# Performance work log

Measured on AMD Instinct MI355X. Metric: run time of the kernel, lower is better.

Reference implementation:

```python
import jax, jax.numpy as jnp
import numpy as np

B, N, D, CI, CO = 16, 1024, 16, 128, 128
ITERS = 3
EPS_BN = 1e-5
EPS_SQ = 1e-8


def sparsemax(z, axis):
    # Martins & Astudillo sparsemax along `axis`.
    K = z.shape[axis]
    z_s = jnp.flip(jnp.sort(z, axis=axis), axis=axis)  # descending
    z_cum = jnp.cumsum(z_s, axis=axis)
    shp = [1] * z.ndim
    shp[axis] = K
    k = jnp.arange(1, K + 1, dtype=z.dtype).reshape(shp)
    support = 1.0 + k * z_s > z_cum
    k_z = jnp.sum(support, axis=axis, keepdims=True).astype(z.dtype)
    tau_sum = jnp.sum(jnp.where(support, z_s, 0.0), axis=axis, keepdims=True)
    tau = (tau_sum - 1.0) / k_z
    return jnp.maximum(z - tau, 0.0)


def squash(s, axis):
    sq = jnp.sum(s * s, axis=axis, keepdims=True)
    return (sq / (1.0 + sq)) * s / jnp.sqrt(sq + EPS_SQ)


def setup_inputs() -> dict:
    key = jax.random.key(0)
    ks = jax.random.split(key, 4)
    x = jax.random.normal(ks[0], (B, N, CI), jnp.float32)
    a = jax.random.uniform(ks[1], (B, N, N), jnp.float32)
    adj = (a < 0.02).astype(jnp.float32)
    adj = jnp.maximum(adj, jnp.swapaxes(adj, -1, -2))  # symmetric 0/1 adjacency
    bn_gamma = jnp.ones((CI,), jnp.float32)
    bn_beta = jnp.zeros((CI,), jnp.float32)
    W = jax.random.normal(ks[2], (D, CI, CO), jnp.float32) / np.sqrt(CI)
    bias = jnp.zeros((D, CO), jnp.float32)
    return {"x": x, "adj": adj, "bn_gamma": bn_gamma, "bn_beta": bn_beta,
            "W": W, "bias": bias}


def _forward(x, adj, bn_gamma, bn_beta, W, bias):
    # BatchNorm1d, training-mode batch stats over flattened [B*N, CI]
    xf = x.reshape(-1, x.shape[-1])
    mu = xf.mean(0)
    var = ((xf - mu) ** 2).mean(0)  # biased variance (torch BN normalization)
    xn = (x - mu) / jnp.sqrt(var + EPS_BN) * bn_gamma + bn_beta

    # DenseGCNConv per digit capsule; adjacency normalization is shared.
    n = adj.shape[-1]
    eye = jnp.eye(n, dtype=adj.dtype)
    a = adj * (1.0 - eye) + eye                    # diag set to 1 (self-loops)
    dis = jnp.clip(a.sum(-1), 1.0, None) ** -0.5
    a_norm = dis[:, :, None] * a * dis[:, None, :]  # D^-1/2 A D^-1/2
    xw = jnp.einsum('bni,dio->bndo', xn, W)
    u = jnp.einsum('bmn,bndo->bmdo', a_norm, xw) + bias  # u_hat [B,N,D,CO]

    u_det = jax.lax.stop_gradient(u)  # torch uses u_hat.detach() in the loop
    b = jnp.zeros(u.shape[:3], u.dtype)  # [B,N,D]
    for _ in range(ITERS - 1):
        c = sparsemax(b, axis=2)
        s = jnp.einsum('bnd,bndo->bdo', c, u_det)
        v = squash(s, axis=-1)  # squash over capsule dim (dim=-2 in torch view)
        b = b + jnp.einsum('bndo,bdo->bnd', u_det, v)

    c = sparsemax(b, axis=2)
    s = jnp.einsum('bnd,bndo->bdo', c, u)
    s = s + xn.mean(1)[:, None, :]  # residual; broadcasts over D (needs CI==CO)
    # Original squashes with dim=-1 over a trailing singleton -> elementwise squash
    sq = s * s
    v = (sq / (1.0 + sq)) * s / jnp.sqrt(sq + EPS_SQ)

    adj_out = jnp.einsum('bnd,bnm,bme->bde', c, adj, c)  # coarsened adjacency
    return v, adj_out


def reference(x, adj, bn_gamma, bn_beta, W, bias):
    return _forward(x, adj, bn_gamma, bn_beta, W, bias)
```

## Files before the change

### kernel.cpp

```cpp
#include <hip/hip_runtime.h>

#define NB 16
#define NN 1024
#define ND 16
#define NCI 128
#define NCO 128
#define BN_ROWS (NB*NN)
#define MAXDEG 128
#define VOFF_ADJ (NB*ND*NCO)

__device__ __forceinline__ void fma4(float4& a, float s, const float4& w) {
    a.x = fmaf(s, w.x, a.x); a.y = fmaf(s, w.y, a.y);
    a.z = fmaf(s, w.z, a.z); a.w = fmaf(s, w.w, a.w);
}
__device__ __forceinline__ void add4(float4& a, const float4& b) {
    a.x += b.x; a.y += b.y; a.z += b.z; a.w += b.w;
}

__global__ __launch_bounds__(256) void k_pre1(const float* __restrict__ x,
                                              float* __restrict__ pbn,
                                              const float* __restrict__ W,
                                              float* __restrict__ Wt) {
    __shared__ float4 ls[8][32], lq[8][32];
    __shared__ float tile[32][33];
    int t = threadIdx.x;
    if (blockIdx.x < 256) {
        int q = t & 31, rg = t >> 5;
        int row0 = blockIdx.x * 64;
        const float4* x4 = (const float4*)x;
        float4 s = make_float4(0, 0, 0, 0), sq = make_float4(0, 0, 0, 0);
        for (int r = rg; r < 64; r += 8) {
            float4 v = x4[(size_t)(row0 + r) * 32 + q];
            s.x += v.x; s.y += v.y; s.z += v.z; s.w += v.w;
            sq.x = fmaf(v.x, v.x, sq.x); sq.y = fmaf(v.y, v.y, sq.y);
            sq.z = fmaf(v.z, v.z, sq.z); sq.w = fmaf(v.w, v.w, sq.w);
        }
        ls[rg][q] = s; lq[rg][q] = sq;
        __syncthreads();
        if (t < 32) {
            float4 a = ls[0][t];
            #pragma unroll
            for (int r = 1; r < 8; ++r) add4(a, ls[r][t]);
            ((float4*)(pbn + (size_t)blockIdx.x * 256))[t] = a;
        } else if (t < 64) {
            int qq = t - 32;
            float4 a = lq[0][qq];
            #pragma unroll
            for (int r = 1; r < 8; ++r) add4(a, lq[r][qq]);
            ((float4*)(pbn + (size_t)blockIdx.x * 256 + 128))[qq] = a;
        }
    } else {
        int d = blockIdx.x - 256;
        int r = t >> 5, cq = t & 31;
        const float* Wd = W + (size_t)d * NCI * NCO;
        float* Wtd = Wt + (size_t)d * NCI * NCO;
        for (int ti = 0; ti < 4; ++ti)
            for (int tj = 0; tj < 4; ++tj) {
                __syncthreads();
                for (int rr = r; rr < 32; rr += 8)
                    tile[rr][cq] = Wd[(size_t)(ti * 32 + rr) * 128 + tj * 32 + cq];
                __syncthreads();
                for (int rr = r; rr < 32; rr += 8)
                    Wtd[(size_t)(tj * 32 + rr) * 128 + ti * 32 + cq] = tile[cq][rr];
            }
    }
}

__global__ __launch_bounds__(256) void k_pre2(const float* __restrict__ adj,
        float* __restrict__ dis, int* __restrict__ nbr_idx, int* __restrict__ nbr_cnt,
        float* __restrict__ selfd, const float* __restrict__ pbn,
        const float* __restrict__ gamma, const float* __restrict__ beta,
        float* __restrict__ ss, float* __restrict__ xm) {
    int t = threadIdx.x;
    if (blockIdx.x < NB * NN) {
        int bm = blockIdx.x;
        int m = bm & (NN - 1);
        const float4* row4 = (const float4*)(adj + (size_t)bm * NN);
        __shared__ int cnt;
        __shared__ int idx[MAXDEG];
        if (t == 0) { cnt = 1; idx[0] = m; }
        __syncthreads();
        float4 v = row4[t];
        int n0 = t * 4;
        float av[4] = {v.x, v.y, v.z, v.w};
        #pragma unroll
        for (int j = 0; j < 4; ++j) {
            int n = n0 + j;
            if (n == m) {
                selfd[bm] = (av[j] > 0.5f) ? 1.f : 0.f;
            } else if (av[j] > 0.5f) {
                int p = atomicAdd(&cnt, 1);
                if (p < MAXDEG) idx[p] = n;
            }
        }
        __syncthreads();
        int c = min(cnt, MAXDEG);
        if (t == 0) {
            nbr_cnt[bm] = c;
            dis[bm] = rsqrtf((float)c);
        }
        for (int k = t; k < c; k += 256) nbr_idx[(size_t)bm * MAXDEG + k] = idx[k];
    } else {
        int b = blockIdx.x - NB * NN;
        if (t < 128) {
            float s = 0.f, sq = 0.f, sb = 0.f;
            for (int blk = 0; blk < 256; ++blk) {
                float v = pbn[(size_t)blk * 256 + t];
                s += v;
                sq += pbn[(size_t)blk * 256 + 128 + t];
                sb += ((blk >> 4) == b) ? v : 0.f;
            }
            float mu = s * (1.f / BN_ROWS);
            float var = sq * (1.f / BN_ROWS) - mu * mu;
            float sc = gamma[t] * rsqrtf(var + 1e-5f);
            float sh = beta[t] - mu * sc;
            if (b == 0) { ss[t] = sc; ss[128 + t] = sh; }
            xm[b * NCI + t] = sb * (1.f / NN) * sc + sh;
        }
    }
}

__global__ void k_y(const float* __restrict__ x, const float* __restrict__ ss,
                    const float* __restrict__ dis, const int* __restrict__ nbr_idx,
                    const int* __restrict__ nbr_cnt, float* __restrict__ y) {
    int l = blockIdx.x;
    int idx0 = l >> 3;
    int b = (l & 7) + ((idx0 >> 10) << 3);
    int m = idx0 & 1023;
    int bm = (b << 10) + m;
    int t = threadIdx.x;
    int q = t & 31, ng = t >> 5;
    __shared__ float sw[MAXDEG];
    __shared__ int sIdx[MAXDEG];
    int cnt = nbr_cnt[bm];
    float dm = dis[bm];
    for (int k = t; k < cnt; k += 128) {
        int n = nbr_idx[(size_t)bm * MAXDEG + k];
        sIdx[k] = n;
        sw[k] = dm * dis[(b << 10) + n];
    }
    __syncthreads();
    const float4* xb = (const float4*)(x + ((size_t)(b << 10)) * NCI);
    float4 acc = make_float4(0, 0, 0, 0);
    float wsum = 0.f;
    for (int k = ng; k < cnt; k += 4) {
        float w = sw[k];
        float4 v = xb[(size_t)sIdx[k] * 32 + q];
        fma4(acc, w, v);
        wsum += w;
    }
    __shared__ float4 lacc[4][32];
    __shared__ float lws[4];
    lacc[ng][q] = acc;
    if (q == 0) lws[ng] = wsum;
    __syncthreads();
    if (t < 32) {
        float4 a = lacc[0][t];
        add4(a, lacc[1][t]); add4(a, lacc[2][t]); add4(a, lacc[3][t]);
        float wst = lws[0] + lws[1] + lws[2] + lws[3];
        float4 sc = ((const float4*)ss)[t];
        float4 sh = ((const float4*)(ss + 128))[t];
        float4 o;
        o.x = sc.x * a.x + sh.x * wst;
        o.y = sc.y * a.y + sh.y * wst;
        o.z = sc.z * a.z + sh.z * wst;
        o.w = sc.w * a.w + sh.w * wst;
        ((float4*)(y + (size_t)bm * NCI))[t] = o;
    }
}

__device__ __forceinline__ void sv_phase(int b, int d, int t, int mode,
    const float* __restrict__ gsrc, const float* __restrict__ pcs,
    const float* __restrict__ W, const float* __restrict__ Wt,
    const float* __restrict__ bias, const float* __restrict__ xm,
    float* __restrict__ hbuf, float* __restrict__ hbb, float* __restrict__ outv,
    float* gl, float4 (*red)[32], float* redf, float* svec, float* vvv,
    float* csum_s, float* scal)
{
    if (mode == 0) {
        int q = t & 31, rg = t >> 5;
        const float4* yb = (const float4*)(gsrc + (((size_t)b) << 10) * NCI);
        float4 s = make_float4(0, 0, 0, 0);
        #pragma unroll 4
        for (int r = rg; r < 1024; r += 8) add4(s, yb[(size_t)r * 32 + q]);
        red[rg][q] = s;
        if (t == 0) *csum_s = 64.f;
        __syncthreads();
        if (t < 32) {
            float4 a = red[0][t];
            #pragma unroll
            for (int r = 1; r < 8; ++r) add4(a, red[r][t]);
            a.x *= (1.f / 16.f); a.y *= (1.f / 16.f);
            a.z *= (1.f / 16.f); a.w *= (1.f / 16.f);
            ((float4*)gl)[t] = a;
        }
        __syncthreads();
    } else {
        int col = t & 127, half = t >> 7;
        float g = 0.f;
        #pragma unroll 4
        for (int ch = half * 16; ch < half * 16 + 16; ++ch)
            g += gsrc[(((size_t)b * 32 + ch) * 16 + d) * NCI + col];
        ((float*)red)[half * 128 + col] = g;
        if (t == 0) {
            float cs = 0.f;
            #pragma unroll
            for (int ch = 0; ch < 32; ++ch) cs += pcs[(b * 32 + ch) * 16 + d];
            *csum_s = cs;
        }
        __syncthreads();
        if (t < 128) gl[t] = ((float*)red)[t] + ((float*)red)[128 + t];
        __syncthreads();
    }

    {
        int q = t & 31, hh = t >> 5;
        const float4* Wd4 = (const float4*)(W + (size_t)d * NCI * NCO);
        float4 acc = make_float4(0, 0, 0, 0);
        for (int i = hh * 16; i < hh * 16 + 16; ++i)
            fma4(acc, gl[i], Wd4[(size_t)i * 32 + q]);
        red[hh][q] = acc;
    }
    __syncthreads();
    if (t < 32) {
        float4 a = red[0][t];
        #pragma unroll
        for (int r = 1; r < 8; ++r) add4(a, red[r][t]);
        float4 b4 = ((const float4*)(bias + d * NCO))[t];
        float cs = *csum_s;
        a.x = fmaf(cs, b4.x, a.x); a.y = fmaf(cs, b4.y, a.y);
        a.z = fmaf(cs, b4.z, a.z); a.w = fmaf(cs, b4.w, a.w);
        ((float4*)svec)[t] = a;
    }
    __syncthreads();

    if (mode == 2) {
        if (t < 128) {
            float sv2 = svec[t] + xm[b * NCO + t];
            float sq = sv2 * sv2;
            outv[(size_t)(b * 16 + d) * NCO + t] = (sq / (1.f + sq)) * sv2 * rsqrtf(sq + 1e-8f);
        }
        return;
    }

    redf[t] = (t < 128) ? svec[t] * svec[t] : 0.f;
    __syncthreads();
    if (t < 64) {
        float val = redf[t] + redf[t + 64] + redf[t + 128] + redf[t + 192];
        #pragma unroll
        for (int m2 = 32; m2 >= 1; m2 >>= 1) val += __shfl_xor(val, m2);
        if (t == 0) *scal = val;
    }
    __syncthreads();
    if (t < 128) {
        float tot = *scal;
        vvv[t] = (tot / (1.f + tot)) * svec[t] * rsqrtf(tot + 1e-8f);
    }
    __syncthreads();

    {
        int q = t & 31, hh = t >> 5;
        const float4* Wt4 = (const float4*)(Wt + (size_t)d * NCI * NCO);
        float4 acc = make_float4(0, 0, 0, 0);
        for (int o = hh * 16; o < hh * 16 + 16; ++o)
            fma4(acc, vvv[o], Wt4[(size_t)o * 32 + q]);
        red[hh][q] = acc;
    }
    redf[t] = (t < 128) ? bias[d * NCO + t] * vvv[t] : 0.f;
    __syncthreads();
    if (t < 32) {
        float4 a = red[0][t];
        #pragma unroll
        for (int r = 1; r < 8; ++r) add4(a, red[r][t]);
        ((float4*)(hbuf + (size_t)(b * 16 + d) * NCI))[t] = a;
    }
    if (t >= 64 && t < 128) {
        int tt = t - 64;
        float val = redf[tt] + redf[tt + 64] + redf[tt + 128] + redf[tt + 192];
        #pragma unroll
        for (int m2 = 32; m2 >= 1; m2 >>= 1) val += __shfl_xor(val, m2);
        if (tt == 0) hbb[b * 16 + d] = val;
    }
}

__global__ __launch_bounds__(256) void k_sv(const float* __restrict__ gsrc,
        const float* __restrict__ pcs, const float* __restrict__ W,
        const float* __restrict__ Wt, const float* __restrict__ bias,
        const float* __restrict__ xm, float* __restrict__ hbuf,
        float* __restrict__ hbb, float* __restrict__ outv, int mode) {
    __shared__ float gl[128], svec[128], vvv[128];
    __shared__ float4 red[8][32];
    __shared__ float redf[256];
    __shared__ float csum_s, scal;
    int l = blockIdx.x, idx0 = l >> 3;
    int b = (l & 7) + ((idx0 >> 4) << 3);
    int d = idx0 & 15;
    sv_phase(b, d, threadIdx.x, mode, gsrc, pcs, W, Wt, bias, xm,
             hbuf, hbb, outv, gl, red, redf, svec, vvv, &csum_s, &scal);
}

__global__ __launch_bounds__(256) void k_bgc(const float* __restrict__ y,
        const float* __restrict__ hbuf, const float* __restrict__ hbb,
        float* __restrict__ blog, float* __restrict__ cglob,
        float* __restrict__ pg, float* __restrict__ pcs,
        float* __restrict__ outz, int first, int last) {
    int l = blockIdx.x, idx0 = l >> 3;
    int b = (l & 7) + ((idx0 >> 5) << 3);
    int j = idx0 & 31;
    int t = threadIdx.x;
    int n0 = j * 32;
    __shared__ __align__(16) float sy[32 * 128];
    __shared__ __align__(16) float sh[16 * 132];
    __shared__ float shb[16];
    __shared__ float scd[32][17];
    {
        const float4* hb4 = (const float4*)(hbuf + (size_t)b * 16 * NCI);
        float4* sh4 = (float4*)sh;
        for (int jj = t; jj < 16 * 32; jj += 256) {
            int row = jj >> 5, col = jj & 31;
            sh4[row * 33 + col] = hb4[row * 32 + col];
        }
        const float4* yb4 = (const float4*)(y + (((size_t)b << 10) + n0) * NCI);
        float4* sy4 = (float4*)sy;
        for (int jj = t; jj < 32 * 32; jj += 256) sy4[jj] = yb4[jj];
        if (t < 16) shb[t] = hbb[b * 16 + t];
    }
    __syncthreads();
    int nsub = t >> 4, d = t & 15;
    #pragma unroll
    for (int nn = nsub; nn < 32; nn += 16) {
        float acc = 0.f;
        const float* yr = &sy[nn * 128];
        const float* hr = &sh[d * 132];
        #pragma unroll 8
        for (int i = 0; i < 128; i += 4) {
            float4 a = *(const float4*)&yr[i];
            float4 h4 = *(const float4*)&hr[i];
            acc = fmaf(a.x, h4.x, acc);
            acc = fmaf(a.y, h4.y, acc);
            acc = fmaf(a.z, h4.z, acc);
            acc = fmaf(a.w, h4.w, acc);
        }
        size_t idx = (((size_t)b << 10) + n0 + nn) * ND + d;
        float bnew = acc + shb[d] + (first ? 0.f : blog[idx]);
        if (!last) blog[idx] = bnew;
        scd[nn][d] = bnew;
    }
    __syncthreads();
    if (t < 32) {
        float z[16], zs[16];
        #pragma unroll
        for (int d2 = 0; d2 < 16; ++d2) { z[d2] = scd[t][d2]; zs[d2] = z[d2]; }
        #pragma unroll
        for (int a = 0; a < 16; ++a) {
            #pragma unroll
            for (int b2 = a + 1; b2 < 16; ++b2) {
                float hi = fmaxf(zs[a], zs[b2]);
                float lo = fminf(zs[a], zs[b2]);
                zs[a] = hi; zs[b2] = lo;
            }
        }
        float cs = 0.f, tausum = 0.f;
        int kz = 1;
        #pragma unroll
        for (int k = 1; k <= 16; ++k) {
            cs += zs[k - 1];
            if (1.f + (float)k * zs[k - 1] > cs) { kz = k; tausum = cs; }
        }
        float tau = (tausum - 1.f) / (float)kz;
        #pragma unroll
        for (int d2 = 0; d2 < 16; ++d2) scd[t][d2] = fmaxf(z[d2] - tau, 0.f);
    }
    __syncthreads();
    if (last) {
        for (int jj = t; jj < 32 * 16; jj += 256)
            cglob[(((size_t)b << 10) + n0 + (jj >> 4)) * ND + (jj & 15)] = scd[jj >> 4][jj & 15];
        if (j == 0) outz[VOFF_ADJ + b * 256 + t] = 0.f;
    }
    if (t < 16) {
        float cs = 0.f;
        #pragma unroll 4
        for (int nn = 0; nn < 32; ++nn) cs += scd[nn][t];
        pcs[(b * 32 + j) * 16 + t] = cs;
    }
    int col = t & 127, dh = t >> 7;
    float accg[8] = {};
    for (int nn = 0; nn < 32; ++nn) {
        float yv = sy[nn * 128 + col];
        #pragma unroll
        for (int dd = 0; dd < 8; ++dd) accg[dd] = fmaf(scd[nn][dh * 8 + dd], yv, accg[dd]);
    }
    #pragma unroll
    for (int dd = 0; dd < 8; ++dd)
        pg[(((size_t)b * 32 + j) * 16 + dh * 8 + dd) * NCI + col] = accg[dd];
}

__global__ __launch_bounds__(256) void k_svt(const float* __restrict__ pg,
        const float* __restrict__ pcs, const float* __restrict__ W,
        const float* __restrict__ Wt, const float* __restrict__ bias,
        const float* __restrict__ xm, float* __restrict__ hbuf,
        float* __restrict__ hbb, const float* __restrict__ cglob,
        const int* __restrict__ nbr_idx, const int* __restrict__ nbr_cnt,
        const float* __restrict__ selfd, float* __restrict__ outv) {
    __shared__ float gl[128], svec[128], vvv[128];
    __shared__ float4 red[8][32];
    __shared__ float redf[256];
    __shared__ float csum_s, scal;
    __shared__ float cm[32][17], tm[32][17];
    int t = threadIdx.x;
    if (blockIdx.x < 256) {
        int l = blockIdx.x, idx0 = l >> 3;
        int b = (l & 7) + ((idx0 >> 4) << 3);
        int d = idx0 & 15;
        sv_phase(b, d, t, 2, pg, pcs, W, Wt, bias, xm,
                 hbuf, hbb, outv, gl, red, redf, svec, vvv, &csum_s, &scal);
        return;
    }
    int l2 = blockIdx.x - 256, idx0 = l2 >> 3;
    int b = (l2 & 7) + ((idx0 >> 5) << 3);
    int j = idx0 & 31;
    for (int jj = t; jj < 32 * 16; jj += 256)
        cm[jj >> 4][jj & 15] = cglob[(((size_t)b << 10) + j * 32 + (jj >> 4)) * ND + (jj & 15)];
    __syncthreads();
    int w = t >> 6, tg = t & 63, nsub = tg >> 4, d = tg & 15;
    for (int mm = w; mm < 32; mm += 4) {
        int m = j * 32 + mm;
        int bm = (b << 10) + m;
        int cnt = nbr_cnt[bm];
        float acc = 0.f;
        for (int k = nsub; k < cnt; k += 4) {
            int n = nbr_idx[(size_t)bm * MAXDEG + k];
            acc += cglob[(((size_t)b << 10) + n) * ND + d];
        }
        acc += __shfl_xor(acc, 16);
        acc += __shfl_xor(acc, 32);
        if (tg < 16) {
            if (selfd[bm] == 0.f) acc -= cm[mm][d];
            tm[mm][d] = acc;
        }
    }
    __syncthreads();
    int d2 = t >> 4, e2 = t & 15;
    float s = 0.f;
    #pragma unroll 8
    for (int mm = 0; mm < 32; ++mm) s = fmaf(tm[mm][d2], cm[mm][e2], s);
    atomicAdd(&outv[VOFF_ADJ + b * 256 + t], s);
}

extern "C" void kernel_launch(void* const* d_in, const int* in_sizes, int n_in,
                              void* d_out, int out_size, void* d_ws, size_t ws_size,
                              hipStream_t stream) {
    const float* x     = (const float*)d_in[0];
    const float* adj   = (const float*)d_in[1];
    const float* gamma = (const float*)d_in[2];
    const float* beta  = (const float*)d_in[3];
    const float* W     = (const float*)d_in[4];
    const float* bias  = (const float*)d_in[5];
    float* out = (float*)d_out;

    char* wptr = (char*)d_ws;
    size_t used = 0;
    auto alloc = [&](size_t nbytes) -> void* {
        void* p = wptr + used;
        used += (nbytes + 255) & ~(size_t)255;
        return p;
    };
    float* pbn     = (float*)alloc((size_t)256 * 256 * 4);
    float* ss      = (float*)alloc(256 * 4);
    float* xm      = (float*)alloc((size_t)NB * NCI * 4);
    float* dis     = (float*)alloc((size_t)NB * NN * 4);
    float* selfd   = (float*)alloc((size_t)NB * NN * 4);
    int*   nbr_cnt = (int*)alloc((size_t)NB * NN * 4);
    float* Wt      = (float*)alloc((size_t)ND * NCI * NCO * 4);
    float* y       = (float*)alloc((size_t)NB * NN * NCI * 4);
    float* blog    = (float*)alloc((size_t)NB * NN * ND * 4);
    float* cglob   = (float*)alloc((size_t)NB * NN * ND * 4);
    float* pg      = (float*)alloc((size_t)NB * 32 * ND * NCI * 4);
    float* pcs     = (float*)alloc((size_t)NB * 32 * ND * 4);
    float* hbuf    = (float*)alloc((size_t)NB * ND * NCI * 4);
    float* hbb     = (float*)alloc((size_t)NB * ND * 4);
    int*   nbr_idx = (int*)alloc((size_t)NB * NN * MAXDEG * 4);
    if (used > ws_size) return;

    k_pre1<<<256 + ND, 256, 0, stream>>>(x, pbn, W, Wt);
    k_pre2<<<NB * NN + NB, 256, 0, stream>>>(adj, dis, nbr_idx, nbr_cnt, selfd,
                                             pbn, gamma, beta, ss, xm);
    k_y<<<NB * NN, 128, 0, stream>>>(x, ss, dis, nbr_idx, nbr_cnt, y);

    k_sv<<<NB * ND, 256, 0, stream>>>(y, pcs, W, Wt, bias, xm, hbuf, hbb, out, 0);
    k_bgc<<<NB * 32, 256, 0, stream>>>(y, hbuf, hbb, blog, cglob, pg, pcs, out, 1, 0);
    k_sv<<<NB * ND, 256, 0, stream>>>(pg, pcs, W, Wt, bias, xm, hbuf, hbb, out, 1);
    k_bgc<<<NB * 32, 256, 0, stream>>>(y, hbuf, hbb, blog, cglob, pg, pcs, out, 0, 1);
    k_svt<<<256 + NB * 32, 256, 0, stream>>>(pg, pcs, W, Wt, bias, xm, hbuf, hbb,
                                             cglob, nbr_idx, nbr_cnt, selfd, out);
}
```

Measured before the change: 138.2 us.

## Merge preprocessing kernels, defer BN affine into consumers, accumulate routing logits in h

Folds the adjacency neighbor-list build into k_pre1 and the BN-stat finalize into the aggregation kernel, cutting one launch and the dependency between BN stats and the y computation. The aggregation now stores raw neighbor sums plus per-row weight sums, and the BN scale/shift is applied later in k_sv and k_bgc. The blog logit buffer is removed: h vectors and biases are accumulated across iterations, since the logits are linear in v. This trades a little extra arithmetic in the consumers for fewer launches and less global traffic.

```diff
diff --git a/kernel.cpp b/kernel.cpp
--- a/kernel.cpp
+++ b/kernel.cpp
@@ -20,9 +20,16 @@
 __global__ __launch_bounds__(256) void k_pre1(const float* __restrict__ x,
                                               float* __restrict__ pbn,
                                               const float* __restrict__ W,
-                                              float* __restrict__ Wt) {
+                                              float* __restrict__ Wt,
+                                              const float* __restrict__ adj,
+                                              float* __restrict__ dis,
+                                              int* __restrict__ nbr_idx,
+                                              int* __restrict__ nbr_cnt,
+                                              float* __restrict__ selfd) {
     __shared__ float4 ls[8][32], lq[8][32];
     __shared__ float tile[32][33];
+    __shared__ int cnt;
+    __shared__ int idx[MAXDEG];
     int t = threadIdx.x;
     if (blockIdx.x < 256) {
         int q = t & 31, rg = t >> 5;
@@ -49,7 +56,7 @@
             for (int r = 1; r < 8; ++r) add4(a, lq[r][qq]);
             ((float4*)(pbn + (size_t)blockIdx.x * 256 + 128))[qq] = a;
         }
-    } else {
+    } else if (blockIdx.x < 272) {
         int d = blockIdx.x - 256;
         int r = t >> 5, cq = t & 31;
         const float* Wd = W + (size_t)d * NCI * NCO;
@@ -63,21 +70,10 @@
                 for (int rr = r; rr < 32; rr += 8)
                     Wtd[(size_t)(tj * 32 + rr) * 128 + ti * 32 + cq] = tile[cq][rr];
             }
-    }
-}
-
-__global__ __launch_bounds__(256) void k_pre2(const float* __restrict__ adj,
-        float* __restrict__ dis, int* __restrict__ nbr_idx, int* __restrict__ nbr_cnt,
-        float* __restrict__ selfd, const float* __restrict__ pbn,
-        const float* __restrict__ gamma, const float* __restrict__ beta,
-        float* __restrict__ ss, float* __restrict__ xm) {
-    int t = threadIdx.x;
-    if (blockIdx.x < NB * NN) {
-        int bm = blockIdx.x;
+    } else {
+        int bm = blockIdx.x - 272;
         int m = bm & (NN - 1);
         const float4* row4 = (const float4*)(adj + (size_t)bm * NN);
-        __shared__ int cnt;
-        __shared__ int idx[MAXDEG];
         if (t == 0) { cnt = 1; idx[0] = m; }
         __syncthreads();
         float4 v = row4[t];
@@ -100,35 +96,38 @@
             dis[bm] = rsqrtf((float)c);
         }
         for (int k = t; k < c; k += 256) nbr_idx[(size_t)bm * MAXDEG + k] = idx[k];
-    } else {
-        int b = blockIdx.x - NB * NN;
-        if (t < 128) {
-            float s = 0.f, sq = 0.f, sb = 0.f;
-            for (int blk = 0; blk < 256; ++blk) {
-                float v = pbn[(size_t)blk * 256 + t];
-                s += v;
-                sq += pbn[(size_t)blk * 256 + 128 + t];
-                sb += ((blk >> 4) == b) ? v : 0.f;
-            }
-            float mu = s * (1.f / BN_ROWS);
-            float var = sq * (1.f / BN_ROWS) - mu * mu;
-            float sc = gamma[t] * rsqrtf(var + 1e-5f);
-            float sh = beta[t] - mu * sc;
-            if (b == 0) { ss[t] = sc; ss[128 + t] = sh; }
-            xm[b * NCI + t] = sb * (1.f / NN) * sc + sh;
-        }
-    }
-}
-
-__global__ void k_y(const float* __restrict__ x, const float* __restrict__ ss,
-                    const float* __restrict__ dis, const int* __restrict__ nbr_idx,
-                    const int* __restrict__ nbr_cnt, float* __restrict__ y) {
-    int l = blockIdx.x;
+    }
+}
+
+__global__ void k_pre2(const float* __restrict__ x, const float* __restrict__ dis,
+                       const int* __restrict__ nbr_idx, const int* __restrict__ nbr_cnt,
+                       float* __restrict__ yraw, float* __restrict__ wsum,
+                       const float* __restrict__ pbn, const float* __restrict__ gamma,
+                       const float* __restrict__ beta, float* __restrict__ ss,
+                       float* __restrict__ xm) {
+    int t = threadIdx.x;
+    if (blockIdx.x < 16) {
+        int b = blockIdx.x;
+        float s = 0.f, sq = 0.f, sb = 0.f;
+        for (int blk = 0; blk < 256; ++blk) {
+            float v = pbn[(size_t)blk * 256 + t];
+            s += v;
+            sq += pbn[(size_t)blk * 256 + 128 + t];
+            sb += ((blk >> 4) == b) ? v : 0.f;
+        }
+        float mu = s * (1.f / BN_ROWS);
+        float var = sq * (1.f / BN_ROWS) - mu * mu;
+        float sc = gamma[t] * rsqrtf(var + 1e-5f);
+        float sh = beta[t] - mu * sc;
+        if (b == 0) { ss[t] = sc; ss[128 + t] = sh; }
+        xm[b * NCI + t] = sb * (1.f / NN) * sc + sh;
+        return;
+    }
+    int l = blockIdx.x - 16;
     int idx0 = l >> 3;
     int b = (l & 7) + ((idx0 >> 10) << 3);
     int m = idx0 & 1023;
     int bm = (b << 10) + m;
-    int t = threadIdx.x;
     int q = t & 31, ng = t >> 5;
     __shared__ float sw[MAXDEG];
     __shared__ int sIdx[MAXDEG];
@@ -142,35 +141,29 @@
     __syncthreads();
     const float4* xb = (const float4*)(x + ((size_t)(b << 10)) * NCI);
     float4 acc = make_float4(0, 0, 0, 0);
-    float wsum = 0.f;
+    float ws = 0.f;
     for (int k = ng; k < cnt; k += 4) {
         float w = sw[k];
         float4 v = xb[(size_t)sIdx[k] * 32 + q];
         fma4(acc, w, v);
-        wsum += w;
+        ws += w;
     }
     __shared__ float4 lacc[4][32];
     __shared__ float lws[4];
     lacc[ng][q] = acc;
-    if (q == 0) lws[ng] = wsum;
+    if (q == 0) lws[ng] = ws;
     __syncthreads();
     if (t < 32) {
         float4 a = lacc[0][t];
         add4(a, lacc[1][t]); add4(a, lacc[2][t]); add4(a, lacc[3][t]);
-        float wst = lws[0] + lws[1] + lws[2] + lws[3];
-        float4 sc = ((const float4*)ss)[t];
-        float4 sh = ((const float4*)(ss + 128))[t];
-        float4 o;
-        o.x = sc.x * a.x + sh.x * wst;
-        o.y = sc.y * a.y + sh.y * wst;
-        o.z = sc.z * a.z + sh.z * wst;
-        o.w = sc.w * a.w + sh.w * wst;
-        ((float4*)(y + (size_t)bm * NCI))[t] = o;
-    }
-}
-
-__device__ __forceinline__ void sv_phase(int b, int d, int t, int mode,
-    const float* __restrict__ gsrc, const float* __restrict__ pcs,
+        ((float4*)(yraw + (size_t)bm * NCI))[t] = a;
+        if (t == 0) wsum[bm] = lws[0] + lws[1] + lws[2] + lws[3];
+    }
+}
+
+__device__ __forceinline__ void sv_phase(int b, int d, int t, int mode, int haccum,
+    const float* __restrict__ gsrc, const float* __restrict__ wsum,
+    const float* __restrict__ ss, const float* __restrict__ pcs,
     const float* __restrict__ W, const float* __restrict__ Wt,
     const float* __restrict__ bias, const float* __restrict__ xm,
     float* __restrict__ hbuf, float* __restrict__ hbb, float* __restrict__ outv,
@@ -184,15 +177,26 @@
         #pragma unroll 4
         for (int r = rg; r < 1024; r += 8) add4(s, yb[(size_t)r * 32 + q]);
         red[rg][q] = s;
+        float w = 0.f;
+        for (int r = t; r < 1024; r += 256) w += wsum[(b << 10) + r];
+        redf[t] = w;
         if (t == 0) *csum_s = 64.f;
         __syncthreads();
         if (t < 32) {
             float4 a = red[0][t];
             #pragma unroll
             for (int r = 1; r < 8; ++r) add4(a, red[r][t]);
-            a.x *= (1.f / 16.f); a.y *= (1.f / 16.f);
-            a.z *= (1.f / 16.f); a.w *= (1.f / 16.f);
-            ((float4*)gl)[t] = a;
+            float wst = 0.f;
+            #pragma unroll 8
+            for (int i = 0; i < 256; ++i) wst += redf[i];
+            float4 sc = ((const float4*)ss)[t];
+            float4 sh = ((const float4*)(ss + 128))[t];
+            float4 g;
+            g.x = (sc.x * a.x + sh.x * wst) * (1.f / 16.f);
+            g.y = (sc.y * a.y + sh.y * wst) * (1.f / 16.f);
+            g.z = (sc.z * a.z + sh.z * wst) * (1.f / 16.f);
+            g.w = (sc.w * a.w + sh.w * wst) * (1.f / 16.f);
+            ((float4*)gl)[t] = g;
         }
         __syncthreads();
     } else {
@@ -272,22 +276,25 @@
         float4 a = red[0][t];
         #pragma unroll
         for (int r = 1; r < 8; ++r) add4(a, red[r][t]);
-        ((float4*)(hbuf + (size_t)(b * 16 + d) * NCI))[t] = a;
+        float4* hp = (float4*)(hbuf + (size_t)(b * 16 + d) * NCI);
+        if (haccum) add4(a, hp[t]);
+        hp[t] = a;
     }
     if (t >= 64 && t < 128) {
         int tt = t - 64;
         float val = redf[tt] + redf[tt + 64] + redf[tt + 128] + redf[tt + 192];
         #pragma unroll
         for (int m2 = 32; m2 >= 1; m2 >>= 1) val += __shfl_xor(val, m2);
-        if (tt == 0) hbb[b * 16 + d] = val;
+        if (tt == 0) hbb[b * 16 + d] = haccum ? (hbb[b * 16 + d] + val) : val;
     }
 }
 
 __global__ __launch_bounds__(256) void k_sv(const float* __restrict__ gsrc,
+        const float* __restrict__ wsum, const float* __restrict__ ss,
         const float* __restrict__ pcs, const float* __restrict__ W,
         const float* __restrict__ Wt, const float* __restrict__ bias,
         const float* __restrict__ xm, float* __restrict__ hbuf,
-        float* __restrict__ hbb, float* __restrict__ outv, int mode) {
+        float* __restrict__ hbb, float* __restrict__ outv, int mode, int haccum) {
     __shared__ float gl[128], svec[128], vvv[128];
     __shared__ float4 red[8][32];
     __shared__ float redf[256];
@@ -295,15 +302,15 @@
     int l = blockIdx.x, idx0 = l >> 3;
     int b = (l & 7) + ((idx0 >> 4) << 3);
     int d = idx0 & 15;
-    sv_phase(b, d, threadIdx.x, mode, gsrc, pcs, W, Wt, bias, xm,
+    sv_phase(b, d, threadIdx.x, mode, haccum, gsrc, wsum, ss, pcs, W, Wt, bias, xm,
              hbuf, hbb, outv, gl, red, redf, svec, vvv, &csum_s, &scal);
 }
 
-__global__ __launch_bounds__(256) void k_bgc(const float* __restrict__ y,
+__global__ __launch_bounds__(256) void k_bgc(const float* __restrict__ yraw,
+        const float* __restrict__ wsum, const float* __restrict__ ss,
         const float* __restrict__ hbuf, const float* __restrict__ hbb,
-        float* __restrict__ blog, float* __restrict__ cglob,
-        float* __restrict__ pg, float* __restrict__ pcs,
-        float* __restrict__ outz, int first, int last) {
+        float* __restrict__ cglob, float* __restrict__ pg, float* __restrict__ pcs,
+        float* __restrict__ outz, int last) {
     int l = blockIdx.x, idx0 = l >> 3;
     int b = (l & 7) + ((idx0 >> 5) << 3);
     int j = idx0 & 31;
@@ -311,19 +318,39 @@
     int n0 = j * 32;
     __shared__ __align__(16) float sy[32 * 128];
     __shared__ __align__(16) float sh[16 * 132];
+    __shared__ float sss[256];
+    __shared__ float swn[32];
     __shared__ float shb[16];
     __shared__ float scd[32][17];
     {
+        if (t < 256) sss[t] = ss[t];
+        if (t < 32) swn[t] = wsum[((size_t)b << 10) + n0 + t];
+        if (t < 16) shb[t] = hbb[b * 16 + t];
         const float4* hb4 = (const float4*)(hbuf + (size_t)b * 16 * NCI);
         float4* sh4 = (float4*)sh;
         for (int jj = t; jj < 16 * 32; jj += 256) {
             int row = jj >> 5, col = jj & 31;
             sh4[row * 33 + col] = hb4[row * 32 + col];
         }
-        const float4* yb4 = (const float4*)(y + (((size_t)b << 10) + n0) * NCI);
+    }
+    __syncthreads();
+    {
+        const float4* yb4 = (const float4*)(yraw + (((size_t)b << 10) + n0) * NCI);
         float4* sy4 = (float4*)sy;
-        for (int jj = t; jj < 32 * 32; jj += 256) sy4[jj] = yb4[jj];
-        if (t < 16) shb[t] = hbb[b * 16 + t];
+        const float4* sc4 = (const float4*)sss;
+        const float4* sh4p = (const float4*)(sss + 128);
+        for (int jj = t; jj < 32 * 32; jj += 256) {
+            int row = jj >> 5, col = jj & 31;
+            float4 v = yb4[jj];
+            float4 sc = sc4[col], shf = sh4p[col];
+            float wn = swn[row];
+            float4 o;
+            o.x = sc.x * v.x + shf.x * wn;
+            o.y = sc.y * v.y + shf.y * wn;
+            o.z = sc.z * v.z + shf.z * wn;
+            o.w = sc.w * v.w + shf.w * wn;
+            sy4[jj] = o;
+        }
     }
     __syncthreads();
     int nsub = t >> 4, d = t & 15;
@@ -341,10 +368,7 @@
             acc = fmaf(a.z, h4.z, acc);
             acc = fmaf(a.w, h4.w, acc);
         }
-        size_t idx = (((size_t)b << 10) + n0 + nn) * ND + d;
-        float bnew = acc + shb[d] + (first ? 0.f : blog[idx]);
-        if (!last) blog[idx] = bnew;
-        scd[nn][d] = bnew;
+        scd[nn][d] = acc + shb[d];
     }
     __syncthreads();
     if (t < 32) {
@@ -412,7 +436,7 @@
         int l = blockIdx.x, idx0 = l >> 3;
         int b = (l & 7) + ((idx0 >> 4) << 3);
         int d = idx0 & 15;
-        sv_phase(b, d, t, 2, pg, pcs, W, Wt, bias, xm,
+        sv_phase(b, d, t, 2, 0, pg, pg, pg, pcs, W, Wt, bias, xm,
                  hbuf, hbb, outv, gl, red, redf, svec, vvv, &csum_s, &scal);
         return;
     }
@@ -472,8 +496,8 @@
     float* selfd   = (float*)alloc((size_t)NB * NN * 4);
     int*   nbr_cnt = (int*)alloc((size_t)NB * NN * 4);
     float* Wt      = (float*)alloc((size_t)ND * NCI * NCO * 4);
-    float* y       = (float*)alloc((size_t)NB * NN * NCI * 4);
-    float* blog    = (float*)alloc((size_t)NB * NN * ND * 4);
+    float* yraw    = (float*)alloc((size_t)NB * NN * NCI * 4);
+    float* wsum    = (float*)alloc((size_t)NB * NN * 4);
     float* cglob   = (float*)alloc((size_t)NB * NN * ND * 4);
     float* pg      = (float*)alloc((size_t)NB * 32 * ND * NCI * 4);
     float* pcs     = (float*)alloc((size_t)NB * 32 * ND * 4);
@@ -482,15 +506,16 @@
     int*   nbr_idx = (int*)alloc((size_t)NB * NN * MAXDEG * 4);
     if (used > ws_size) return;
 
-    k_pre1<<<256 + ND, 256, 0, stream>>>(x, pbn, W, Wt);
-    k_pre2<<<NB * NN + NB, 256, 0, stream>>>(adj, dis, nbr_idx, nbr_cnt, selfd,
+    k_pre1<<<272 + NB * NN, 256, 0, stream>>>(x, pbn, W, Wt, adj, dis,
+                                              nbr_idx, nbr_cnt, selfd);
+    k_pre2<<<16 + NB * NN, 128, 0, stream>>>(x, dis, nbr_idx, nbr_cnt, yraw, wsum,
                                              pbn, gamma, beta, ss, xm);
-    k_y<<<NB * NN, 128, 0, stream>>>(x, ss, dis, nbr_idx, nbr_cnt, y);
-
-    k_sv<<<NB * ND, 256, 0, stream>>>(y, pcs, W, Wt, bias, xm, hbuf, hbb, out, 0);
-    k_bgc<<<NB * 32, 256, 0, stream>>>(y, hbuf, hbb, blog, cglob, pg, pcs, out, 1, 0);
-    k_sv<<<NB * ND, 256, 0, stream>>>(pg, pcs, W, Wt, bias, xm, hbuf, hbb, out, 1);
-    k_bgc<<<NB * 32, 256, 0, stream>>>(y, hbuf, hbb, blog, cglob, pg, pcs, out, 0, 1);
+    k_sv<<<NB * ND, 256, 0, stream>>>(yraw, wsum, ss, pcs, W, Wt, bias, xm,
+                                      hbuf, hbb, out, 0, 0);
+    k_bgc<<<NB * 32, 256, 0, stream>>>(yraw, wsum, ss, hbuf, hbb, cglob, pg, pcs, out, 0);
+    k_sv<<<NB * ND, 256, 0, stream>>>(pg, wsum, ss, pcs, W, Wt, bias, xm,
+                                      hbuf, hbb, out, 1, 1);
+    k_bgc<<<NB * 32, 256, 0, stream>>>(yraw, wsum, ss, hbuf, hbb, cglob, pg, pcs, out, 1);
     k_svt<<<256 + NB * 32, 256, 0, stream>>>(pg, pcs, W, Wt, bias, xm, hbuf, hbb,
                                              cglob, nbr_idx, nbr_cnt, selfd, out);
 }
```

After: 128.1 us. 1.08x faster.
